# Kernel tuning notes

Hardware: AMD Instinct MI355X
Metric: run time of the kernel (lower is better)

## Reference

```python
import jax, jax.numpy as jnp
import numpy as np

N = 8192
F_IN, F_HID, F_OUT = 256, 256, 64


def setup_inputs() -> dict:
    key = jax.random.key(0)
    k1, k2, k3, k4 = jax.random.split(key, 4)
    adj = jax.random.uniform(k1, (N, N), dtype=jnp.float32)
    x = jax.random.normal(k2, (N, F_IN), dtype=jnp.float32)
    W1 = jax.random.uniform(k3, (F_IN, F_HID), dtype=jnp.float32)
    W2 = jax.random.uniform(k4, (F_HID, F_OUT), dtype=jnp.float32)
    return {"adj": adj, "x": x, "W1": W1, "W2": W2}


def reference(adj, x, W1, W2):
    # Layer 1: left_to_right -> (adj @ x) @ W1, then ReLU (dropout is identity in eval)
    h = jnp.matmul(jnp.matmul(adj, x), W1)
    h = jax.nn.relu(h)
    # Layer 2 (last): no activation
    h = jnp.matmul(jnp.matmul(adj, h), W2)
    # Final log_softmax over class dim
    return jax.nn.log_softmax(h, axis=1)
```

## Files before the change

kernel.cpp:

```cpp
#include <hip/hip_runtime.h>

typedef short bf16x8 __attribute__((ext_vector_type(8)));
typedef float f32x4 __attribute__((ext_vector_type(4)));
typedef unsigned short us8 __attribute__((ext_vector_type(8)));

__device__ __forceinline__ unsigned short f2bf(float f) {
    unsigned int u = __float_as_uint(f);
    u += 0x7fffu + ((u >> 16) & 1u);
    return (unsigned short)(u >> 16);
}
__device__ __forceinline__ float bf2f(unsigned short s) {
    return __uint_as_float((unsigned int)s << 16);
}

__device__ __forceinline__ void hard_barrier() {
    asm volatile("s_waitcnt lgkmcnt(0)" ::: "memory");
    __builtin_amdgcn_sched_barrier(0);
    __builtin_amdgcn_s_barrier();
    __builtin_amdgcn_sched_barrier(0);
}

__device__ __forceinline__ void transpose_tile(
    const float* __restrict__ in, unsigned short* __restrict__ out,
    int R, int Cc, int r0, int c0, int t) {
    __shared__ alignas(16) unsigned short sT[64][65];
#pragma unroll
    for (int p = 0; p < 16; ++p) {
        int flat = p * 256 + t;
        int r = flat >> 6, c = flat & 63;
        sT[c][r] = f2bf(in[(size_t)(r0 + r) * Cc + (c0 + c)]);
    }
    __syncthreads();
#pragma unroll
    for (int p = 0; p < 16; ++p) {
        int flat = p * 256 + t;
        int c = flat >> 6, r = flat & 63;
        out[(size_t)(c0 + c) * R + (r0 + r)] = sT[c][r];
    }
}

__global__ __launch_bounds__(256) void transpose2_kernel(
    const float* __restrict__ W1, const float* __restrict__ W2,
    unsigned short* __restrict__ W1T, unsigned short* __restrict__ W2T) {
    const int bx = blockIdx.x, t = threadIdx.x;
    if (bx < 16) transpose_tile(W1, W1T, 256, 256, (bx & 3) * 64, (bx >> 2) * 64, t);
    else         transpose_tile(W2, W2T, 256, 64, (bx - 16) * 64, 0, t);
}

template<int BN, int WM, int WN, int AMODE, bool TOUT, typename OutT>
__global__ __launch_bounds__(256) void gemm_kernel(
    const void* __restrict__ Aptr, const unsigned short* __restrict__ BT,
    OutT* __restrict__ C, int M, int N, int K, long aslab) {
    constexpr int BM = 64, BK = 64, LDW = 72;
    constexpr int MF = BM / WM / 16;
    constexpr int NF = BN / WN / 16;
    __shared__ alignas(16) unsigned short sA[BM * LDW];
    __shared__ alignas(16) unsigned short sB[BN * LDW];
    const int t = threadIdx.x;
    const int w = t >> 6, l = t & 63;
    const int wr = w / WN, wc = w % WN;
    const int m0 = blockIdx.x * BM;

    f32x4 acc[MF][NF] = {};

    for (int k0 = 0; k0 < K; k0 += BK) {
        if constexpr (AMODE == 1) {
            const float* A32 = (const float*)Aptr;
#pragma unroll
            for (int p = 0; p < 4; ++p) {
                int flat = p * 256 + t;
                int row = flat >> 4, c4 = flat & 15;
                float4 v = *(const float4*)&A32[(size_t)(m0 + row) * K + k0 + c4 * 4];
                *(ushort4*)&sA[row * LDW + c4 * 4] =
                    make_ushort4(f2bf(v.x), f2bf(v.y), f2bf(v.z), f2bf(v.w));
            }
        } else {
            const unsigned short* A16 = (const unsigned short*)Aptr;
#pragma unroll
            for (int p = 0; p < 2; ++p) {
                int flat = p * 256 + t;
                int row = flat >> 3, c8 = flat & 7;
                size_t base = (size_t)(m0 + row) * K + k0 + c8 * 8;
                float s[8] = {};
#pragma unroll
                for (int sl = 0; sl < 4; ++sl) {
                    us8 v = *(const us8*)&A16[(size_t)sl * aslab + base];
#pragma unroll
                    for (int e = 0; e < 8; ++e) s[e] += bf2f(v[e]);
                }
                us8 o;
#pragma unroll
                for (int e = 0; e < 8; ++e) o[e] = f2bf(fmaxf(s[e], 0.f));
                *(us8*)&sA[row * LDW + c8 * 8] = o;
            }
        }
#pragma unroll
        for (int p = 0; p < BN * 8 / 256; ++p) {
            int flat = p * 256 + t;
            int row = flat >> 3, c8 = flat & 7;
            us8 v = *(const us8*)&BT[(size_t)row * K + k0 + c8 * 8];
            *(us8*)&sB[row * LDW + c8 * 8] = v;
        }
        __syncthreads();
#pragma unroll
        for (int kk = 0; kk < BK; kk += 32) {
            bf16x8 av[MF], bv[NF];
#pragma unroll
            for (int m = 0; m < MF; ++m)
                av[m] = *(const bf16x8*)&sA[(wr * (BM / WM) + m * 16 + (l & 15)) * LDW + kk + (l >> 4) * 8];
#pragma unroll
            for (int n = 0; n < NF; ++n)
                bv[n] = *(const bf16x8*)&sB[(wc * (BN / WN) + n * 16 + (l & 15)) * LDW + kk + (l >> 4) * 8];
#pragma unroll
            for (int m = 0; m < MF; ++m)
#pragma unroll
                for (int n = 0; n < NF; ++n)
                    acc[m][n] = __builtin_amdgcn_mfma_f32_16x16x32_bf16(av[m], bv[n], acc[m][n], 0, 0, 0);
        }
        __syncthreads();
    }

#pragma unroll
    for (int m = 0; m < MF; ++m) {
#pragma unroll
        for (int n = 0; n < NF; ++n) {
            const int col = wc * (BN / WN) + n * 16 + (l & 15);
            const int rb = m0 + wr * (BM / WM) + m * 16 + ((l >> 4) << 2);
            float v0 = acc[m][n][0], v1 = acc[m][n][1], v2 = acc[m][n][2], v3 = acc[m][n][3];
            if constexpr (TOUT) {
                ushort4 o = make_ushort4(f2bf(v0), f2bf(v1), f2bf(v2), f2bf(v3));
                *(ushort4*)((unsigned short*)C + (size_t)col * M + rb) = o;
            } else {
                C[(size_t)(rb + 0) * N + col] = (OutT)v0;
                C[(size_t)(rb + 1) * N + col] = (OutT)v1;
                C[(size_t)(rb + 2) * N + col] = (OutT)v2;
                C[(size_t)(rb + 3) * N + col] = (OutT)v3;
            }
        }
    }
}

template<int BM, int BN, int WM, int WN, int THREADS, int MINB, bool OUTBF>
__global__ __launch_bounds__(THREADS, MINB) void pipe_gemm_kernel(
    const float* __restrict__ A, const unsigned short* __restrict__ BT,
    void* __restrict__ Cout, int M, int N, int K) {
    constexpr int BK = 64, LDW = 72;
    constexpr int MF = BM / WM / 16, NF = BN / WN / 16;
    constexpr int ACH = BM * BK / 4 / THREADS;
    constexpr int BCH = BN * BK / 8 / THREADS;
    static_assert(ACH * THREADS * 4 == BM * BK && BCH * THREADS * 8 == BN * BK, "split");
    __shared__ alignas(16) unsigned short sA[2][BM * LDW];
    __shared__ alignas(16) unsigned short sB[2][BN * LDW];
    const int t = threadIdx.x, w = t >> 6, l = t & 63;
    const int wr = w / WN, wc = w % WN;
    const int nx = gridDim.x;
    const int lin = blockIdx.x + nx * blockIdx.z;
    const int cpx = (nx * gridDim.z) >> 3;
    const int sw = (lin & 7) * cpx + (lin >> 3);
    const int bx = sw % nx, bz = sw / nx;
    const int m0 = bx * BM;
    const int klen = K / gridDim.z, kbeg = bz * klen;
    const int NT = klen / BK;

    float4 a0[ACH], a1[ACH];
    us8 b0[BCH], b1[BCH];

    auto LOAD = [&](float4 (&ar)[ACH], us8 (&br)[BCH], int k0) {
#pragma unroll
        for (int p = 0; p < ACH; ++p) {
            int flat = p * THREADS + t, row = flat >> 4, c4 = flat & 15;
            ar[p] = *(const float4*)&A[(size_t)(m0 + row) * K + k0 + c4 * 4];
        }
#pragma unroll
        for (int p = 0; p < BCH; ++p) {
            int flat = p * THREADS + t, row = flat >> 3, c8 = flat & 7;
            br[p] = *(const us8*)&BT[(size_t)row * K + k0 + c8 * 8];
        }
    };
    auto WRITE = [&](float4 (&ar)[ACH], us8 (&br)[BCH], int buf) {
#pragma unroll
        for (int p = 0; p < ACH; ++p) {
            int flat = p * THREADS + t, row = flat >> 4, c4 = flat & 15;
            float4 v = ar[p];
            *(ushort4*)&sA[buf][row * LDW + c4 * 4] =
                make_ushort4(f2bf(v.x), f2bf(v.y), f2bf(v.z), f2bf(v.w));
        }
#pragma unroll
        for (int p = 0; p < BCH; ++p) {
            int flat = p * THREADS + t, row = flat >> 3, c8 = flat & 7;
            *(us8*)&sB[buf][row * LDW + c8 * 8] = br[p];
        }
    };

    f32x4 acc[MF][NF] = {};

    auto COMPUTE = [&](int buf) {
#pragma unroll
        for (int kk = 0; kk < BK; kk += 32) {
            bf16x8 av[MF], bv[NF];
#pragma unroll
            for (int m = 0; m < MF; ++m)
                av[m] = *(const bf16x8*)&sA[buf][(wr * (BM / WM) + m * 16 + (l & 15)) * LDW + kk + (l >> 4) * 8];
#pragma unroll
            for (int n = 0; n < NF; ++n)
                bv[n] = *(const bf16x8*)&sB[buf][(wc * (BN / WN) + n * 16 + (l & 15)) * LDW + kk + (l >> 4) * 8];
#pragma unroll
            for (int m = 0; m < MF; ++m)
#pragma unroll
                for (int n = 0; n < NF; ++n)
                    acc[m][n] = __builtin_amdgcn_mfma_f32_16x16x32_bf16(av[m], bv[n], acc[m][n], 0, 0, 0);
        }
    };

    LOAD(a0, b0, kbeg);
    LOAD(a1, b1, kbeg + BK);
    WRITE(a0, b0, 0);
    hard_barrier();

    for (int tt = 0; tt < NT; tt += 2) {
        if (tt + 2 < NT) LOAD(a0, b0, kbeg + (tt + 2) * BK);
        __builtin_amdgcn_sched_barrier(0);
        COMPUTE(0);
        if (tt + 1 < NT) WRITE(a1, b1, 1);
        hard_barrier();
        if (tt + 1 < NT) {
            if (tt + 3 < NT) LOAD(a1, b1, kbeg + (tt + 3) * BK);
            __builtin_amdgcn_sched_barrier(0);
            COMPUTE(1);
            if (tt + 2 < NT) WRITE(a0, b0, 0);
            hard_barrier();
        }
    }

#pragma unroll
    for (int m = 0; m < MF; ++m)
#pragma unroll
        for (int n = 0; n < NF; ++n) {
            const int col = wc * (BN / WN) + n * 16 + (l & 15);
            const int rb = m0 + wr * (BM / WM) + m * 16 + ((l >> 4) << 2);
#pragma unroll
            for (int j = 0; j < 4; ++j) {
                if constexpr (OUTBF)
                    ((unsigned short*)Cout)[(size_t)bz * M * N + (size_t)(rb + j) * N + col] =
                        f2bf(acc[m][n][j]);
                else
                    ((float*)Cout)[(size_t)bz * M * N + (size_t)(rb + j) * N + col] =
                        acc[m][n][j];
            }
        }
}

__global__ __launch_bounds__(256) void head2_kernel(
    const float* __restrict__ p, float* __restrict__ out, int M) {
    const int t = threadIdx.x, w = t >> 6, l = t & 63;
    const size_t stride = (size_t)M * 64;
#pragma unroll
    for (int rr = 0; rr < 4; ++rr) {
        int i = blockIdx.x * 16 + w * 4 + rr;
        size_t off = (size_t)i * 64 + l;
        float v = 0.f;
#pragma unroll
        for (int s = 0; s < 8; ++s) v += p[s * stride + off];
        float mx = v;
#pragma unroll
        for (int o = 32; o; o >>= 1) mx = fmaxf(mx, __shfl_xor(mx, o));
        float d0 = v - mx;
        float e = __expf(d0);
#pragma unroll
        for (int o = 32; o; o >>= 1) e += __shfl_xor(e, o);
        out[off] = d0 - __logf(e);
    }
}

extern "C" void kernel_launch(void* const* d_in, const int* in_sizes, int n_in,
                              void* d_out, int out_size, void* d_ws, size_t ws_size,
                              hipStream_t stream) {
    const float* adj = (const float*)d_in[0];
    const float* x   = (const float*)d_in[1];
    const float* W1  = (const float*)d_in[2];
    const float* W2  = (const float*)d_in[3];
    float* out = (float*)d_out;

    const int M = 8192, K = 8192;
    char* ws = (char*)d_ws;
    unsigned short* pbuf1 = (unsigned short*)ws;
    float*          pbuf2 = (float*)(ws + 16777216);
    unsigned short* zT    = (unsigned short*)(ws + 33554432);
    unsigned short* hwT   = (unsigned short*)(ws + 37748736);
    unsigned short* W1T   = (unsigned short*)(ws + 38797312);
    unsigned short* W2T   = (unsigned short*)(ws + 38928384);

    transpose2_kernel<<<dim3(20), 256, 0, stream>>>(W1, W2, W1T, W2T);
    gemm_kernel<256, 1, 4, 1, true, unsigned short>
        <<<dim3(M / 64), 256, 0, stream>>>(x, W1T, zT, M, 256, 256, 0);
    pipe_gemm_kernel<128, 256, 4, 4, 1024, 1, true>
        <<<dim3(M / 128, 1, 4), 1024, 0, stream>>>(adj, zT, pbuf1, M, 256, K);
    gemm_kernel<64, 2, 2, 4, true, unsigned short>
        <<<dim3(M / 64), 256, 0, stream>>>(pbuf1, W2T, hwT, M, 64, 256, (long)M * 256);
    pipe_gemm_kernel<128, 64, 4, 2, 512, 2, false>
        <<<dim3(M / 128, 1, 8), 512, 0, stream>>>(adj, hwT, pbuf2, M, 64, K);
    head2_kernel<<<dim3(M / 16), 256, 0, stream>>>(pbuf2, out, M);
}
```

Measured before the change: 149.8 us.

## Load B fragments directly from global memory instead of staging through LDS

Removes the shared-memory double buffer for the bf16 B operand and has each wave read its MFMA B fragments straight from global memory during compute. This cuts LDS footprint and the LDS write/read traffic for B, and may raise occupancy. In exchange, global load latency now sits inside the compute step without prefetching, and different waves reload the same B data redundantly through the caches.

```diff
diff --git a/kernel.cpp b/kernel.cpp
--- a/kernel.cpp
+++ b/kernel.cpp
@@ -147,10 +147,8 @@
     constexpr int BK = 64, LDW = 72;
     constexpr int MF = BM / WM / 16, NF = BN / WN / 16;
     constexpr int ACH = BM * BK / 4 / THREADS;
-    constexpr int BCH = BN * BK / 8 / THREADS;
-    static_assert(ACH * THREADS * 4 == BM * BK && BCH * THREADS * 8 == BN * BK, "split");
+    static_assert(ACH * THREADS * 4 == BM * BK, "split");
     __shared__ alignas(16) unsigned short sA[2][BM * LDW];
-    __shared__ alignas(16) unsigned short sB[2][BN * LDW];
     const int t = threadIdx.x, w = t >> 6, l = t & 63;
     const int wr = w / WN, wc = w % WN;
     const int nx = gridDim.x;
@@ -163,21 +161,15 @@
     const int NT = klen / BK;
 
     float4 a0[ACH], a1[ACH];
-    us8 b0[BCH], b1[BCH];
-
-    auto LOAD = [&](float4 (&ar)[ACH], us8 (&br)[BCH], int k0) {
+
+    auto LOAD = [&](float4 (&ar)[ACH], int k0) {
 #pragma unroll
         for (int p = 0; p < ACH; ++p) {
             int flat = p * THREADS + t, row = flat >> 4, c4 = flat & 15;
             ar[p] = *(const float4*)&A[(size_t)(m0 + row) * K + k0 + c4 * 4];
         }
-#pragma unroll
-        for (int p = 0; p < BCH; ++p) {
-            int flat = p * THREADS + t, row = flat >> 3, c8 = flat & 7;
-            br[p] = *(const us8*)&BT[(size_t)row * K + k0 + c8 * 8];
-        }
     };
-    auto WRITE = [&](float4 (&ar)[ACH], us8 (&br)[BCH], int buf) {
+    auto WRITE = [&](float4 (&ar)[ACH], int buf) {
 #pragma unroll
         for (int p = 0; p < ACH; ++p) {
             int flat = p * THREADS + t, row = flat >> 4, c4 = flat & 15;
@@ -185,25 +177,25 @@
             *(ushort4*)&sA[buf][row * LDW + c4 * 4] =
                 make_ushort4(f2bf(v.x), f2bf(v.y), f2bf(v.z), f2bf(v.w));
         }
-#pragma unroll
-        for (int p = 0; p < BCH; ++p) {
-            int flat = p * THREADS + t, row = flat >> 3, c8 = flat & 7;
-            *(us8*)&sB[buf][row * LDW + c8 * 8] = br[p];
-        }
     };
 
     f32x4 acc[MF][NF] = {};
 
-    auto COMPUTE = [&](int buf) {
+    const unsigned short* brow[NF];
+#pragma unroll
+    for (int n = 0; n < NF; ++n)
+        brow[n] = &BT[(size_t)(wc * (BN / WN) + n * 16 + (l & 15)) * K + (l >> 4) * 8];
+
+    auto COMPUTE = [&](int buf, int k0) {
 #pragma unroll
         for (int kk = 0; kk < BK; kk += 32) {
             bf16x8 av[MF], bv[NF];
 #pragma unroll
+            for (int n = 0; n < NF; ++n)
+                bv[n] = *(const bf16x8*)&brow[n][k0 + kk];
+#pragma unroll
             for (int m = 0; m < MF; ++m)
                 av[m] = *(const bf16x8*)&sA[buf][(wr * (BM / WM) + m * 16 + (l & 15)) * LDW + kk + (l >> 4) * 8];
-#pragma unroll
-            for (int n = 0; n < NF; ++n)
-                bv[n] = *(const bf16x8*)&sB[buf][(wc * (BN / WN) + n * 16 + (l & 15)) * LDW + kk + (l >> 4) * 8];
 #pragma unroll
             for (int m = 0; m < MF; ++m)
 #pragma unroll
@@ -212,22 +204,22 @@
         }
     };
 
-    LOAD(a0, b0, kbeg);
-    LOAD(a1, b1, kbeg + BK);
-    WRITE(a0, b0, 0);
+    LOAD(a0, kbeg);
+    LOAD(a1, kbeg + BK);
+    WRITE(a0, 0);
     hard_barrier();
 
     for (int tt = 0; tt < NT; tt += 2) {
-        if (tt + 2 < NT) LOAD(a0, b0, kbeg + (tt + 2) * BK);
+        if (tt + 2 < NT) LOAD(a0, kbeg + (tt + 2) * BK);
         __builtin_amdgcn_sched_barrier(0);
-        COMPUTE(0);
-        if (tt + 1 < NT) WRITE(a1, b1, 1);
+        COMPUTE(0, kbeg + tt * BK);
+        if (tt + 1 < NT) WRITE(a1, 1);
         hard_barrier();
         if (tt + 1 < NT) {
-            if (tt + 3 < NT) LOAD(a1, b1, kbeg + (tt + 3) * BK);
+            if (tt + 3 < NT) LOAD(a1, kbeg + (tt + 3) * BK);
             __builtin_amdgcn_sched_barrier(0);
-            COMPUTE(1);
-            if (tt + 2 < NT) WRITE(a0, b0, 0);
+            COMPUTE(1, kbeg + (tt + 1) * BK);
+            if (tt + 2 < NT) WRITE(a0, 0);
             hard_barrier();
         }
     }
```

After: 251.5 us. 67.9% more time.
